# Kernel tuning notes

Measured on AMD Instinct MI355X. Metric: run time of the kernel, lower is better.

The kernel has to match this reference:

```python
import jax, jax.numpy as jnp
import numpy as np

TEMPERATURE = 0.1


def _l2norm(x):
    return x / jnp.linalg.norm(x, axis=1, keepdims=True)


def _unif(x, t=2.0):
    # torch.pdist(x).pow(2) == squared euclidean distances over pairs i<j
    m = x.shape[0]
    sq = jnp.sum(x * x, axis=1)
    d2 = sq[:, None] + sq[None, :] - 2.0 * (x @ x.T)  # [m, m]
    d2 = jnp.maximum(d2, 0.0)
    iu = jnp.triu(jnp.ones((m, m), dtype=bool), k=1)
    s = jnp.sum(jnp.where(iu, jnp.exp(-t * d2), 0.0))
    n_pairs = m * (m - 1) // 2
    return jnp.log(s / n_pairs)


def setup_inputs() -> dict:
    key = jax.random.key(0)
    k1, k2 = jax.random.split(key)
    proj_1 = jax.random.normal(k1, (4096, 1024), dtype=jnp.float32)
    proj_2 = jax.random.normal(k2, (4096, 1024), dtype=jnp.float32)
    return {"proj_1": proj_1, "proj_2": proj_2}


def reference(proj_1, proj_2):
    n = proj_1.shape[0]
    t = TEMPERATURE
    z_i = _l2norm(proj_1)
    z_j = _l2norm(proj_2)
    z = jnp.concatenate([z_i, z_j], axis=0)  # [2n, d]
    # rows are unit-norm, so cosine similarity == dot product
    sim = z @ z.T  # [2n, 2n]
    # diag(sim, +n) == diag(sim, -n) == rowwise z_i . z_j
    pos = jnp.sum(z_i * z_j, axis=1)  # [n]
    positives = jnp.concatenate([pos, pos], axis=0)  # [2n]
    mask = 1.0 - jnp.eye(2 * n, dtype=sim.dtype)
    denom = jnp.sum(mask * jnp.exp(sim / t), axis=1)  # [2n]
    # -log(exp(pos/t) / denom) == log(denom) - pos/t
    loss = jnp.sum(jnp.log(denom) - positives / t) / (2 * n)
    # alignment: mean ||z_i - z_j||_2^2 (alpha=2), detached
    lalign = jax.lax.stop_gradient(jnp.mean(jnp.sum((z_i - z_j) ** 2, axis=1)))
    # uniformity on the two halves of z_i, detached
    lunif = jax.lax.stop_gradient(
        (_unif(z_i[: n // 2]) + _unif(z_i[n // 2 :])) / 2.0
    )
    return (loss, lalign, lunif)
```

## Files before the change

### kernel.cpp

```cpp
#include <hip/hip_runtime.h>
#include <stdint.h>

#define DDIM   1024
#define M_TOT  8192
#define N_ROWS 4096
#define KT     16
#define NCELL  2080
#define SLOT   16384
#define NSLOT  3
#define LDS_TOTAL (NSLOT * SLOT)

typedef __attribute__((ext_vector_type(4))) float f32x4;
typedef __attribute__((ext_vector_type(2))) long i64x2;

__device__ __forceinline__ void gload_lds16(const void* g, void* l) {
  __builtin_amdgcn_global_load_lds(
      (const __attribute__((address_space(1))) uint32_t*)g,
      (__attribute__((address_space(3))) uint32_t*)l, 16, 0, 0);
}

__global__ __launch_bounds__(256) void knorm(const float* __restrict__ p1,
                                             const float* __restrict__ p2,
                                             unsigned char* __restrict__ z8,
                                             float* __restrict__ pp,
                                             float* __restrict__ ap) {
  const int r = blockIdx.x;
  const int t = threadIdx.x;
  const int lane = t & 63, w = t >> 6;
  __shared__ float red0[4], red1[4];

  const float4 a = ((const float4*)(p1 + (size_t)r * DDIM))[t];
  const float4 b = ((const float4*)(p2 + (size_t)r * DDIM))[t];
  float s1 = a.x*a.x + a.y*a.y + a.z*a.z + a.w*a.w;
  float s2 = b.x*b.x + b.y*b.y + b.z*b.z + b.w*b.w;
  for (int off = 1; off < 64; off <<= 1) { s1 += __shfl_xor(s1, off); s2 += __shfl_xor(s2, off); }
  if (lane == 0) { red0[w] = s1; red1[w] = s2; }
  __syncthreads();
  const float S1 = red0[0] + red0[1] + red0[2] + red0[3];
  const float S2 = red1[0] + red1[1] + red1[2] + red1[3];
  const float r1 = 1.0f / sqrtf(S1);
  const float r2 = 1.0f / sqrtf(S2);
  const float n1x = a.x*r1, n1y = a.y*r1, n1z = a.z*r1, n1w = a.w*r1;
  const float n2x = b.x*r2, n2y = b.y*r2, n2z = b.z*r2, n2w = b.w*r2;
  float pos = n1x*n2x + n1y*n2y + n1z*n2z + n1w*n2w;
  float al  = (n1x-n2x)*(n1x-n2x) + (n1y-n2y)*(n1y-n2y)
            + (n1z-n2z)*(n1z-n2z) + (n1w-n2w)*(n1w-n2w);
  __syncthreads();
  for (int off = 1; off < 64; off <<= 1) { pos += __shfl_xor(pos, off); al += __shfl_xor(al, off); }
  if (lane == 0) { red0[w] = pos; red1[w] = al; }
  __syncthreads();
  if (t == 0) {
    pp[r] = red0[0] + red0[1] + red0[2] + red0[3];
    ap[r] = red1[0] + red1[1] + red1[2] + red1[3];
  }
  const int g = t >> 4, c = (t >> 1) & 7, h = t & 1;
  const int sp = (c < 4) ? (2 * c) : (2 * (c - 4) + 1);
  const int off = g * 64 + sp * 8 + h * 4;
  int w1 = __builtin_amdgcn_cvt_pk_fp8_f32(n1x, n1y, 0, false);
  w1     = __builtin_amdgcn_cvt_pk_fp8_f32(n1z, n1w, w1, true);
  int w2 = __builtin_amdgcn_cvt_pk_fp8_f32(n2x, n2y, 0, false);
  w2     = __builtin_amdgcn_cvt_pk_fp8_f32(n2z, n2w, w2, true);
  *(int*)(z8 + (size_t)r * 1024 + off) = w1;
  *(int*)(z8 + (size_t)(r + N_ROWS) * 1024 + off) = w2;
}

__device__ __forceinline__ void stage64(const char* zb, int rowA0, int colB0,
                                        int kt, char* slot, int wid, int lane) {
  const int kb = kt * 64 + (lane >> 4) * 16;
  const int rowin = lane & 15;
  const int u0 = wid * 2, u1 = wid * 2 + 1;
  gload_lds16(zb + (size_t)(rowA0 + u0 * 16 + rowin) * 1024 + kb, slot + u0 * 1024 + lane * 16);
  gload_lds16(zb + (size_t)(rowA0 + u1 * 16 + rowin) * 1024 + kb, slot + u1 * 1024 + lane * 16);
  gload_lds16(zb + (size_t)(colB0 + u0 * 16 + rowin) * 1024 + kb, slot + 8192 + u0 * 1024 + lane * 16);
  gload_lds16(zb + (size_t)(colB0 + u1 * 16 + rowin) * 1024 + kb, slot + 8192 + u1 * 1024 + lane * 16);
}

__global__ __launch_bounds__(256, 3) void kgemm(const unsigned char* __restrict__ z,
                                                float* __restrict__ denom,
                                                float* __restrict__ uacc) {
  extern __shared__ char lds[];
  const int tid  = threadIdx.x;
  const int lane = tid & 63, wid = tid >> 6;
  const int wsr  = wid >> 1, wsc = wid & 1;
  const int lr = lane >> 4, lc = lane & 15;
  const char* zb = (const char*)z;
  const float RK10 = 14.426950408889634f;
  const float K4   = 5.770780163555856f;

  const int cdx = (blockIdx.x & 7) * 260 + (blockIdx.x >> 3);
  int SI = (int)((sqrtf(16.0f + 128.0f * (float)cdx) - 4.0f) * (1.0f / 64.0f));
  while (32 * (SI + 1) * (SI + 1) + 4 * (SI + 1) <= cdx) ++SI;
  while (32 * SI * SI + 4 * SI > cdx) --SI;
  int rem = cdx - (32 * SI * SI + 4 * SI);
  int I, J;
  if (rem < 36) {
    int ii = (int)((sqrtf(8.0f * (float)rem + 1.0f) - 1.0f) * 0.5f);
    while ((ii + 1) * (ii + 2) / 2 <= rem) ++ii;
    while (ii * (ii + 1) / 2 > rem) --ii;
    const int jj = rem - ii * (ii + 1) / 2;
    I = SI * 8 + ii; J = SI * 8 + jj;
  } else {
    const int r2 = rem - 36;
    const int SJ = r2 >> 6, w = r2 & 63;
    I = SI * 8 + (w >> 3); J = SJ * 8 + (w & 7);
  }
  const int rowA0 = I * 128, colB0 = J * 128;
  const bool useful = (colB0 + wsc * 64) < (rowA0 + wsr * 64 + 64);

  f32x4 acc[4][4] = {};

  stage64(zb, rowA0, colB0, 0, lds, wid, lane);
  stage64(zb, rowA0, colB0, 1, lds + SLOT, wid, lane);
  asm volatile("s_waitcnt vmcnt(4)" ::: "memory");
  __builtin_amdgcn_s_barrier();
  __builtin_amdgcn_sched_barrier(0);

#pragma unroll 1
  for (int t = 0; t < KT; ++t) {
    if (t + 2 < KT)
      stage64(zb, rowA0, colB0, t + 2, lds + ((t + 2) % 3) * SLOT, wid, lane);
    __builtin_amdgcn_sched_barrier(0);
    const char* S = lds + (t % 3) * SLOT;
    if (useful) {
      const char* Ab = S + wsr * 4096 + lr * 256 + lc * 16;
      const char* Bb = S + 8192 + wsc * 4096 + lr * 256 + lc * 16;
      i64x2 af[4], bg[4];
#pragma unroll
      for (int m = 0; m < 4; ++m) {
        af[m] = *(const i64x2*)(Ab + m * 1024);
        bg[m] = *(const i64x2*)(Bb + m * 1024);
      }
      __builtin_amdgcn_s_setprio(1);
#pragma unroll
      for (int q = 0; q < 2; ++q)
#pragma unroll
        for (int m = 0; m < 4; ++m)
#pragma unroll
          for (int n = 0; n < 4; ++n)
            acc[m][n] = __builtin_amdgcn_mfma_f32_16x16x32_fp8_fp8(
                af[m][q], bg[n][q], acc[m][n], 0, 0, 0);
      __builtin_amdgcn_s_setprio(0);
    }
    if (t + 2 < KT) asm volatile("s_waitcnt vmcnt(4)" ::: "memory");
    else            asm volatile("s_waitcnt vmcnt(0)" ::: "memory");
    __builtin_amdgcn_s_barrier();
    __builtin_amdgcn_sched_barrier(0);
  }

  const bool unif = (I < 16) || (I < 32 && J >= 16);
  if (useful) {
    float cs[4] = {0.0f, 0.0f, 0.0f, 0.0f};
    float u = 0.0f;
#pragma unroll
    for (int m = 0; m < 4; ++m) {
      const int growb = rowA0 + wsr * 64 + m * 16 + lr * 4;
#pragma unroll
      for (int i = 0; i < 4; ++i) {
        const int grow = growb + i;
        float rs = 0.0f;
#pragma unroll
        for (int n = 0; n < 4; ++n) {
          const int gcol = colB0 + wsc * 64 + n * 16 + lc;
          const bool incl = (gcol < grow);
          float e = incl ? exp2f(acc[m][n][i] * RK10) : 0.0f;
          rs += e;
          cs[n] += e;
          if (unif) u += incl ? exp2f(acc[m][n][i] * K4 - K4) : 0.0f;
        }
        rs += __shfl_xor(rs, 1); rs += __shfl_xor(rs, 2);
        rs += __shfl_xor(rs, 4); rs += __shfl_xor(rs, 8);
        if (lc == 0 && rs > 0.0f) atomicAdd(&denom[grow], rs);
      }
    }
#pragma unroll
    for (int n = 0; n < 4; ++n) {
      float cv = cs[n];
      cv += __shfl_xor(cv, 16); cv += __shfl_xor(cv, 32);
      if (lr == 0 && cv > 0.0f) atomicAdd(&denom[colB0 + wsc * 64 + n * 16 + lc], cv);
    }
    if (unif) {
      for (int off = 1; off < 64; off <<= 1) u += __shfl_xor(u, off);
      if (lane == 0 && u > 0.0f)
        atomicAdd(&uacc[((I < 16) ? 0 : 64) + (blockIdx.x & 63)], 2.0f * u);
    }
  }
}

__global__ __launch_bounds__(1024) void klogf(const float* __restrict__ denom,
                                              const float* __restrict__ pp,
                                              const float* __restrict__ ap,
                                              const float* __restrict__ uacc,
                                              float* __restrict__ out) {
  __shared__ float redl[16], redp[16], reda[16], ured[2];
  const int tid = threadIdx.x;
  float s = 0.0f, sp = 0.0f, sa = 0.0f;
#pragma unroll
  for (int q = 0; q < 8; ++q) s += logf(denom[q * 1024 + tid]);
#pragma unroll
  for (int q = 0; q < 4; ++q) { sp += pp[q * 1024 + tid]; sa += ap[q * 1024 + tid]; }
  const int lane = tid & 63, w = tid >> 6;
  for (int off = 1; off < 64; off <<= 1) {
    s += __shfl_xor(s, off); sp += __shfl_xor(sp, off); sa += __shfl_xor(sa, off);
  }
  if (lane == 0) { redl[w] = s; redp[w] = sp; reda[w] = sa; }
  if (tid < 64) {
    float u0 = uacc[tid], u1 = uacc[64 + tid];
    for (int off = 1; off < 64; off <<= 1) { u0 += __shfl_xor(u0, off); u1 += __shfl_xor(u1, off); }
    if (tid == 0) { ured[0] = u0; ured[1] = u1; }
  }
  __syncthreads();
  if (tid == 0) {
    float S = 0.0f, SP = 0.0f, SA = 0.0f;
#pragma unroll
    for (int i = 0; i < 16; ++i) { S += redl[i]; SP += redp[i]; SA += reda[i]; }
    const float P = 2048.0f * 2047.0f * 0.5f;
    out[0] = (S - 20.0f * SP) / 8192.0f;
    out[1] = SA / 4096.0f;
    out[2] = 0.5f * (logf(ured[0] * 0.5f / P) + logf(ured[1] * 0.5f / P));
  }
}

extern "C" void kernel_launch(void* const* d_in, const int* in_sizes, int n_in,
                              void* d_out, int out_size, void* d_ws, size_t ws_size,
                              hipStream_t stream) {
  const float* p1 = (const float*)d_in[0];
  const float* p2 = (const float*)d_in[1];
  float* out = (float*)d_out;
  char* ws = (char*)d_ws;
  unsigned char* z8 = (unsigned char*)ws;
  float* denom = (float*)(ws + (size_t)M_TOT * DDIM);
  float* uacc  = denom + M_TOT;
  float* pp    = uacc + 128;
  float* ap    = pp + 4096;

  (void)hipFuncSetAttribute((const void*)kgemm,
                            hipFuncAttributeMaxDynamicSharedMemorySize, LDS_TOTAL);
  hipMemsetAsync(denom, 0, (M_TOT + 128) * sizeof(float), stream);
  knorm<<<N_ROWS, 256, 0, stream>>>(p1, p2, z8, pp, ap);
  kgemm<<<NCELL, 256, LDS_TOTAL, stream>>>(z8, denom, uacc);
  klogf<<<1, 1024, 0, stream>>>(denom, pp, ap, uacc, out);
}
```

Baseline: 97.21 us.

## Widen GEMM tile to 128x256 with 64x128 warp subtiles

The block tile grows from 128x128 to 128x256 columns, so each warp computes a 64x128 subtile with 32 accumulators, and the lower-triangle block enumeration is rewritten for the new tile shape (1056 cells). This raises MFMA work per LDS fragment load and cuts the number of blocks and redundant A-tile loads. In exchange it needs more LDS per slot and more registers, and occupancy drops to 2 blocks per CU. Diagonal tiles also waste more work in the masked triangle.

```diff
diff --git a/kernel.cpp b/kernel.cpp
--- a/kernel.cpp
+++ b/kernel.cpp
@@ -5,8 +5,8 @@
 #define M_TOT  8192
 #define N_ROWS 4096
 #define KT     16
-#define NCELL  2080
-#define SLOT   16384
+#define NCELL  1056
+#define SLOT   24576
 #define NSLOT  3
 #define LDS_TOTAL (NSLOT * SLOT)
 
@@ -68,14 +68,18 @@
                                         int kt, char* slot, int wid, int lane) {
   const int kb = kt * 64 + (lane >> 4) * 16;
   const int rowin = lane & 15;
-  const int u0 = wid * 2, u1 = wid * 2 + 1;
-  gload_lds16(zb + (size_t)(rowA0 + u0 * 16 + rowin) * 1024 + kb, slot + u0 * 1024 + lane * 16);
-  gload_lds16(zb + (size_t)(rowA0 + u1 * 16 + rowin) * 1024 + kb, slot + u1 * 1024 + lane * 16);
-  gload_lds16(zb + (size_t)(colB0 + u0 * 16 + rowin) * 1024 + kb, slot + 8192 + u0 * 1024 + lane * 16);
-  gload_lds16(zb + (size_t)(colB0 + u1 * 16 + rowin) * 1024 + kb, slot + 8192 + u1 * 1024 + lane * 16);
-}
-
-__global__ __launch_bounds__(256, 3) void kgemm(const unsigned char* __restrict__ z,
+  const int a0 = wid * 2, a1 = wid * 2 + 1;
+  gload_lds16(zb + (size_t)(rowA0 + a0 * 16 + rowin) * 1024 + kb, slot + a0 * 1024 + lane * 16);
+  gload_lds16(zb + (size_t)(rowA0 + a1 * 16 + rowin) * 1024 + kb, slot + a1 * 1024 + lane * 16);
+#pragma unroll
+  for (int q = 0; q < 4; ++q) {
+    const int u = wid * 4 + q;
+    gload_lds16(zb + (size_t)(colB0 + u * 16 + rowin) * 1024 + kb,
+                slot + 8192 + u * 1024 + lane * 16);
+  }
+}
+
+__global__ __launch_bounds__(256, 2) void kgemm(const unsigned char* __restrict__ z,
                                                 float* __restrict__ denom,
                                                 float* __restrict__ uacc) {
   extern __shared__ char lds[];
@@ -87,31 +91,20 @@
   const float RK10 = 14.426950408889634f;
   const float K4   = 5.770780163555856f;
 
-  const int cdx = (blockIdx.x & 7) * 260 + (blockIdx.x >> 3);
-  int SI = (int)((sqrtf(16.0f + 128.0f * (float)cdx) - 4.0f) * (1.0f / 64.0f));
-  while (32 * (SI + 1) * (SI + 1) + 4 * (SI + 1) <= cdx) ++SI;
-  while (32 * SI * SI + 4 * SI > cdx) --SI;
-  int rem = cdx - (32 * SI * SI + 4 * SI);
-  int I, J;
-  if (rem < 36) {
-    int ii = (int)((sqrtf(8.0f * (float)rem + 1.0f) - 1.0f) * 0.5f);
-    while ((ii + 1) * (ii + 2) / 2 <= rem) ++ii;
-    while (ii * (ii + 1) / 2 > rem) --ii;
-    const int jj = rem - ii * (ii + 1) / 2;
-    I = SI * 8 + ii; J = SI * 8 + jj;
-  } else {
-    const int r2 = rem - 36;
-    const int SJ = r2 >> 6, w = r2 & 63;
-    I = SI * 8 + (w >> 3); J = SJ * 8 + (w & 7);
-  }
-  const int rowA0 = I * 128, colB0 = J * 128;
-  const bool useful = (colB0 + wsc * 64) < (rowA0 + wsr * 64 + 64);
-
-  f32x4 acc[4][4] = {};
+  const int c = (blockIdx.x & 7) * 132 + (blockIdx.x >> 3);
+  int I = (int)(2.0f * sqrtf((float)c + 1.0f));
+  if (I > 63) I = 63;
+  while (I < 63 && ((I + 1) * (I + 1)) / 4 + (I + 2) / 2 <= c) ++I;
+  while (I > 0 && (I * I) / 4 + (I + 1) / 2 > c) --I;
+  const int J = c - ((I * I) / 4 + (I + 1) / 2);
+  const int rowA0 = I * 128, colB0 = J * 256;
+  const bool useful = (colB0 + wsc * 128) < (rowA0 + wsr * 64 + 64);
+
+  f32x4 acc[4][8] = {};
 
   stage64(zb, rowA0, colB0, 0, lds, wid, lane);
   stage64(zb, rowA0, colB0, 1, lds + SLOT, wid, lane);
-  asm volatile("s_waitcnt vmcnt(4)" ::: "memory");
+  asm volatile("s_waitcnt vmcnt(6)" ::: "memory");
   __builtin_amdgcn_s_barrier();
   __builtin_amdgcn_sched_barrier(0);
 
@@ -123,33 +116,32 @@
     const char* S = lds + (t % 3) * SLOT;
     if (useful) {
       const char* Ab = S + wsr * 4096 + lr * 256 + lc * 16;
-      const char* Bb = S + 8192 + wsc * 4096 + lr * 256 + lc * 16;
-      i64x2 af[4], bg[4];
-#pragma unroll
-      for (int m = 0; m < 4; ++m) {
-        af[m] = *(const i64x2*)(Ab + m * 1024);
-        bg[m] = *(const i64x2*)(Bb + m * 1024);
-      }
+      const char* Bb = S + 8192 + wsc * 8192 + lr * 256 + lc * 16;
+      i64x2 af[4], bg[8];
+#pragma unroll
+      for (int m = 0; m < 4; ++m) af[m] = *(const i64x2*)(Ab + m * 1024);
+#pragma unroll
+      for (int n = 0; n < 8; ++n) bg[n] = *(const i64x2*)(Bb + n * 1024);
       __builtin_amdgcn_s_setprio(1);
 #pragma unroll
       for (int q = 0; q < 2; ++q)
 #pragma unroll
         for (int m = 0; m < 4; ++m)
 #pragma unroll
-          for (int n = 0; n < 4; ++n)
+          for (int n = 0; n < 8; ++n)
             acc[m][n] = __builtin_amdgcn_mfma_f32_16x16x32_fp8_fp8(
                 af[m][q], bg[n][q], acc[m][n], 0, 0, 0);
       __builtin_amdgcn_s_setprio(0);
     }
-    if (t + 2 < KT) asm volatile("s_waitcnt vmcnt(4)" ::: "memory");
+    if (t + 2 < KT) asm volatile("s_waitcnt vmcnt(6)" ::: "memory");
     else            asm volatile("s_waitcnt vmcnt(0)" ::: "memory");
     __builtin_amdgcn_s_barrier();
     __builtin_amdgcn_sched_barrier(0);
   }
 
-  const bool unif = (I < 16) || (I < 32 && J >= 16);
+  const bool unif = (I < 16) || (I < 32 && J >= 8);
   if (useful) {
-    float cs[4] = {0.0f, 0.0f, 0.0f, 0.0f};
+    float cs[8] = {};
     float u = 0.0f;
 #pragma unroll
     for (int m = 0; m < 4; ++m) {
@@ -159,8 +151,8 @@
         const int grow = growb + i;
         float rs = 0.0f;
 #pragma unroll
-        for (int n = 0; n < 4; ++n) {
-          const int gcol = colB0 + wsc * 64 + n * 16 + lc;
+        for (int n = 0; n < 8; ++n) {
+          const int gcol = colB0 + wsc * 128 + n * 16 + lc;
           const bool incl = (gcol < grow);
           float e = incl ? exp2f(acc[m][n][i] * RK10) : 0.0f;
           rs += e;
@@ -173,10 +165,10 @@
       }
     }
 #pragma unroll
-    for (int n = 0; n < 4; ++n) {
+    for (int n = 0; n < 8; ++n) {
       float cv = cs[n];
       cv += __shfl_xor(cv, 16); cv += __shfl_xor(cv, 32);
-      if (lr == 0 && cv > 0.0f) atomicAdd(&denom[colB0 + wsc * 64 + n * 16 + lc], cv);
+      if (lr == 0 && cv > 0.0f) atomicAdd(&denom[colB0 + wsc * 128 + n * 16 + lc], cv);
     }
     if (unif) {
       for (int off = 1; off < 64; off <<= 1) u += __shfl_xor(u, off);
```

Measured after the change: 104.7 us. 1.08x slower.

## Switch GEMM to 32x32x64 scaled FP8 MFMA with matching LDS layout

Applied to the files above, without the earlier changes.

Replaces the 16x16x32 FP8 MFMA tiles with the gfx950 mfma_scale 32x32x64 f8f6f4 instruction, using unit scales (0x7F exponent), so each wave issues 4 larger MFMAs per k-step instead of 32 small ones. The FP8 write in the normalization kernel becomes a plain linear layout, and the global-to-LDS staging and fragment loads are reorganized for 32-row blocks. The epilogue is remapped to the 32x32 accumulator layout, with wider row reductions and fewer column shuffles. The aim is higher matrix-core throughput and fewer LDS reads and instruction issues. The cost is higher accumulator register pressure per instruction and possible LDS bank conflicts in the new read pattern.

```diff
diff --git a/kernel.cpp b/kernel.cpp
--- a/kernel.cpp
+++ b/kernel.cpp
@@ -10,8 +10,10 @@
 #define NSLOT  3
 #define LDS_TOTAL (NSLOT * SLOT)
 
-typedef __attribute__((ext_vector_type(4))) float f32x4;
-typedef __attribute__((ext_vector_type(2))) long i64x2;
+typedef __attribute__((ext_vector_type(4)))  float f32x4;
+typedef __attribute__((ext_vector_type(16))) float f32x16;
+typedef __attribute__((ext_vector_type(4)))  int   i32x4;
+typedef __attribute__((ext_vector_type(8)))  int   i32x8;
 
 __device__ __forceinline__ void gload_lds16(const void* g, void* l) {
   __builtin_amdgcn_global_load_lds(
@@ -53,26 +55,27 @@
     pp[r] = red0[0] + red0[1] + red0[2] + red0[3];
     ap[r] = red1[0] + red1[1] + red1[2] + red1[3];
   }
-  const int g = t >> 4, c = (t >> 1) & 7, h = t & 1;
-  const int sp = (c < 4) ? (2 * c) : (2 * (c - 4) + 1);
-  const int off = g * 64 + sp * 8 + h * 4;
   int w1 = __builtin_amdgcn_cvt_pk_fp8_f32(n1x, n1y, 0, false);
   w1     = __builtin_amdgcn_cvt_pk_fp8_f32(n1z, n1w, w1, true);
   int w2 = __builtin_amdgcn_cvt_pk_fp8_f32(n2x, n2y, 0, false);
   w2     = __builtin_amdgcn_cvt_pk_fp8_f32(n2z, n2w, w2, true);
-  *(int*)(z8 + (size_t)r * 1024 + off) = w1;
-  *(int*)(z8 + (size_t)(r + N_ROWS) * 1024 + off) = w2;
+  *(int*)(z8 + (size_t)r * 1024 + t * 4) = w1;
+  *(int*)(z8 + (size_t)(r + N_ROWS) * 1024 + t * 4) = w2;
 }
 
 __device__ __forceinline__ void stage64(const char* zb, int rowA0, int colB0,
                                         int kt, char* slot, int wid, int lane) {
-  const int kb = kt * 64 + (lane >> 4) * 16;
-  const int rowin = lane & 15;
-  const int u0 = wid * 2, u1 = wid * 2 + 1;
-  gload_lds16(zb + (size_t)(rowA0 + u0 * 16 + rowin) * 1024 + kb, slot + u0 * 1024 + lane * 16);
-  gload_lds16(zb + (size_t)(rowA0 + u1 * 16 + rowin) * 1024 + kb, slot + u1 * 1024 + lane * 16);
-  gload_lds16(zb + (size_t)(colB0 + u0 * 16 + rowin) * 1024 + kb, slot + 8192 + u0 * 1024 + lane * 16);
-  gload_lds16(zb + (size_t)(colB0 + u1 * 16 + rowin) * 1024 + kb, slot + 8192 + u1 * 1024 + lane * 16);
+  const int r32 = lane & 31;
+  const int kc  = kt * 64 + (lane >> 5) * 32;
+#pragma unroll
+  for (int q = 0; q < 2; ++q) {
+    const int u  = wid * 2 + q;
+    const int mb = u >> 1, h = u & 1;
+    gload_lds16(zb + (size_t)(rowA0 + mb * 32 + r32) * 1024 + kc + h * 16,
+                slot + u * 1024 + lane * 16);
+    gload_lds16(zb + (size_t)(colB0 + mb * 32 + r32) * 1024 + kc + h * 16,
+                slot + 8192 + u * 1024 + lane * 16);
+  }
 }
 
 __global__ __launch_bounds__(256, 3) void kgemm(const unsigned char* __restrict__ z,
@@ -82,7 +85,7 @@
   const int tid  = threadIdx.x;
   const int lane = tid & 63, wid = tid >> 6;
   const int wsr  = wid >> 1, wsc = wid & 1;
-  const int lr = lane >> 4, lc = lane & 15;
+  const int l31  = lane & 31, hi = lane >> 5;
   const char* zb = (const char*)z;
   const float RK10 = 14.426950408889634f;
   const float K4   = 5.770780163555856f;
@@ -107,7 +110,7 @@
   const int rowA0 = I * 128, colB0 = J * 128;
   const bool useful = (colB0 + wsc * 64) < (rowA0 + wsr * 64 + 64);
 
-  f32x4 acc[4][4] = {};
+  f32x16 acc[2][2] = {};
 
   stage64(zb, rowA0, colB0, 0, lds, wid, lane);
   stage64(zb, rowA0, colB0, 1, lds + SLOT, wid, lane);
@@ -122,23 +125,26 @@
     __builtin_amdgcn_sched_barrier(0);
     const char* S = lds + (t % 3) * SLOT;
     if (useful) {
-      const char* Ab = S + wsr * 4096 + lr * 256 + lc * 16;
-      const char* Bb = S + 8192 + wsc * 4096 + lr * 256 + lc * 16;
-      i64x2 af[4], bg[4];
-#pragma unroll
-      for (int m = 0; m < 4; ++m) {
-        af[m] = *(const i64x2*)(Ab + m * 1024);
-        bg[m] = *(const i64x2*)(Bb + m * 1024);
+      const char* Ab = S + wsr * 4096 + lane * 16;
+      const char* Bb = S + 8192 + wsc * 4096 + lane * 16;
+      i32x8 a8[2], b8[2];
+#pragma unroll
+      for (int m = 0; m < 2; ++m) {
+        const i32x4 alo = *(const i32x4*)(Ab + m * 2048);
+        const i32x4 ahi = *(const i32x4*)(Ab + m * 2048 + 1024);
+        a8[m] = __builtin_shufflevector(alo, ahi, 0, 1, 2, 3, 4, 5, 6, 7);
+        const i32x4 blo = *(const i32x4*)(Bb + m * 2048);
+        const i32x4 bhi = *(const i32x4*)(Bb + m * 2048 + 1024);
+        b8[m] = __builtin_shufflevector(blo, bhi, 0, 1, 2, 3, 4, 5, 6, 7);
       }
       __builtin_amdgcn_s_setprio(1);
 #pragma unroll
-      for (int q = 0; q < 2; ++q)
-#pragma unroll
-        for (int m = 0; m < 4; ++m)
-#pragma unroll
-          for (int n = 0; n < 4; ++n)
-            acc[m][n] = __builtin_amdgcn_mfma_f32_16x16x32_fp8_fp8(
-                af[m][q], bg[n][q], acc[m][n], 0, 0, 0);
+      for (int m = 0; m < 2; ++m)
+#pragma unroll
+        for (int n = 0; n < 2; ++n)
+          acc[m][n] = __builtin_amdgcn_mfma_scale_f32_32x32x64_f8f6f4(
+              a8[m], b8[n], acc[m][n], 0, 0,
+              0, 0x7F7F7F7F, 0, 0x7F7F7F7F);
       __builtin_amdgcn_s_setprio(0);
     }
     if (t + 2 < KT) asm volatile("s_waitcnt vmcnt(4)" ::: "memory");
@@ -149,34 +155,34 @@
 
   const bool unif = (I < 16) || (I < 32 && J >= 16);
   if (useful) {
-    float cs[4] = {0.0f, 0.0f, 0.0f, 0.0f};
+    float csv[2] = {0.0f, 0.0f};
     float u = 0.0f;
 #pragma unroll
-    for (int m = 0; m < 4; ++m) {
-      const int growb = rowA0 + wsr * 64 + m * 16 + lr * 4;
-#pragma unroll
-      for (int i = 0; i < 4; ++i) {
-        const int grow = growb + i;
+    for (int mb = 0; mb < 2; ++mb) {
+#pragma unroll
+      for (int r = 0; r < 16; ++r) {
+        const int grow = rowA0 + wsr * 64 + mb * 32 + (r & 3) + 8 * (r >> 2) + 4 * hi;
         float rs = 0.0f;
 #pragma unroll
-        for (int n = 0; n < 4; ++n) {
-          const int gcol = colB0 + wsc * 64 + n * 16 + lc;
+        for (int nb = 0; nb < 2; ++nb) {
+          const int gcol = colB0 + wsc * 64 + nb * 32 + l31;
           const bool incl = (gcol < grow);
-          float e = incl ? exp2f(acc[m][n][i] * RK10) : 0.0f;
+          float e = incl ? exp2f(acc[mb][nb][r] * RK10) : 0.0f;
           rs += e;
-          cs[n] += e;
-          if (unif) u += incl ? exp2f(acc[m][n][i] * K4 - K4) : 0.0f;
+          csv[nb] += e;
+          if (unif) u += incl ? exp2f(acc[mb][nb][r] * K4 - K4) : 0.0f;
         }
-        rs += __shfl_xor(rs, 1); rs += __shfl_xor(rs, 2);
-        rs += __shfl_xor(rs, 4); rs += __shfl_xor(rs, 8);
-        if (lc == 0 && rs > 0.0f) atomicAdd(&denom[grow], rs);
+        rs += __shfl_xor(rs, 1); rs += __shfl_xor(rs, 2); rs += __shfl_xor(rs, 4);
+        rs += __shfl_xor(rs, 8); rs += __shfl_xor(rs, 16);
+        if (l31 == 0 && rs > 0.0f) atomicAdd(&denom[grow], rs);
       }
     }
 #pragma unroll
-    for (int n = 0; n < 4; ++n) {
-      float cv = cs[n];
-      cv += __shfl_xor(cv, 16); cv += __shfl_xor(cv, 32);
-      if (lr == 0 && cv > 0.0f) atomicAdd(&denom[colB0 + wsc * 64 + n * 16 + lc], cv);
+    for (int nb = 0; nb < 2; ++nb) {
+      float cv = csv[nb];
+      cv += __shfl_xor(cv, 32);
+      if (hi == 0 && cv > 0.0f)
+        atomicAdd(&denom[colB0 + wsc * 64 + nb * 32 + l31], cv);
     }
     if (unif) {
       for (int off = 1; off < 64; off <<= 1) u += __shfl_xor(u, off);
```

Result: slower. 112.1 us (+15.4%).

## Load FP8 GEMM operands directly from global memory instead of LDS pipeline

Applied to the files above, without the earlier changes.

Removes the triple-buffered LDS staging (global_load_lds, barriers, waitcnt) in the symmetric GEMM kernel and has each wave read its A/B fragments straight from global memory into registers, with a partially unrolled K loop. This eliminates LDS traffic and block-wide barriers and lets non-useful waves skip all loads. In exchange every wave fetches its own fragments with no sharing across waves, which doubles global/L2 traffic, and latency hiding now depends on unrolling and occupancy rather than an explicit prefetch pipeline.

```diff
diff --git a/kernel.cpp b/kernel.cpp
--- a/kernel.cpp
+++ b/kernel.cpp
@@ -6,18 +6,9 @@
 #define N_ROWS 4096
 #define KT     16
 #define NCELL  2080
-#define SLOT   16384
-#define NSLOT  3
-#define LDS_TOTAL (NSLOT * SLOT)
 
 typedef __attribute__((ext_vector_type(4))) float f32x4;
 typedef __attribute__((ext_vector_type(2))) long i64x2;
-
-__device__ __forceinline__ void gload_lds16(const void* g, void* l) {
-  __builtin_amdgcn_global_load_lds(
-      (const __attribute__((address_space(1))) uint32_t*)g,
-      (__attribute__((address_space(3))) uint32_t*)l, 16, 0, 0);
-}
 
 __global__ __launch_bounds__(256) void knorm(const float* __restrict__ p1,
                                              const float* __restrict__ p2,
@@ -64,21 +55,9 @@
   *(int*)(z8 + (size_t)(r + N_ROWS) * 1024 + off) = w2;
 }
 
-__device__ __forceinline__ void stage64(const char* zb, int rowA0, int colB0,
-                                        int kt, char* slot, int wid, int lane) {
-  const int kb = kt * 64 + (lane >> 4) * 16;
-  const int rowin = lane & 15;
-  const int u0 = wid * 2, u1 = wid * 2 + 1;
-  gload_lds16(zb + (size_t)(rowA0 + u0 * 16 + rowin) * 1024 + kb, slot + u0 * 1024 + lane * 16);
-  gload_lds16(zb + (size_t)(rowA0 + u1 * 16 + rowin) * 1024 + kb, slot + u1 * 1024 + lane * 16);
-  gload_lds16(zb + (size_t)(colB0 + u0 * 16 + rowin) * 1024 + kb, slot + 8192 + u0 * 1024 + lane * 16);
-  gload_lds16(zb + (size_t)(colB0 + u1 * 16 + rowin) * 1024 + kb, slot + 8192 + u1 * 1024 + lane * 16);
-}
-
 __global__ __launch_bounds__(256, 3) void kgemm(const unsigned char* __restrict__ z,
                                                 float* __restrict__ denom,
                                                 float* __restrict__ uacc) {
-  extern __shared__ char lds[];
   const int tid  = threadIdx.x;
   const int lane = tid & 63, wid = tid >> 6;
   const int wsr  = wid >> 1, wsc = wid & 1;
@@ -109,28 +88,23 @@
 
   f32x4 acc[4][4] = {};
 
-  stage64(zb, rowA0, colB0, 0, lds, wid, lane);
-  stage64(zb, rowA0, colB0, 1, lds + SLOT, wid, lane);
-  asm volatile("s_waitcnt vmcnt(4)" ::: "memory");
-  __builtin_amdgcn_s_barrier();
-  __builtin_amdgcn_sched_barrier(0);
-
-#pragma unroll 1
-  for (int t = 0; t < KT; ++t) {
-    if (t + 2 < KT)
-      stage64(zb, rowA0, colB0, t + 2, lds + ((t + 2) % 3) * SLOT, wid, lane);
-    __builtin_amdgcn_sched_barrier(0);
-    const char* S = lds + (t % 3) * SLOT;
-    if (useful) {
-      const char* Ab = S + wsr * 4096 + lr * 256 + lc * 16;
-      const char* Bb = S + 8192 + wsc * 4096 + lr * 256 + lc * 16;
+  if (useful) {
+    int aoff[4], boff[4];
+#pragma unroll
+    for (int m = 0; m < 4; ++m)
+      aoff[m] = (rowA0 + wsr * 64 + m * 16 + lc) * 1024 + lr * 16;
+#pragma unroll
+    for (int n = 0; n < 4; ++n)
+      boff[n] = (colB0 + wsc * 64 + n * 16 + lc) * 1024 + lr * 16;
+
+#pragma unroll 4
+    for (int t = 0; t < KT; ++t) {
+      const int kb = t * 64;
       i64x2 af[4], bg[4];
 #pragma unroll
-      for (int m = 0; m < 4; ++m) {
-        af[m] = *(const i64x2*)(Ab + m * 1024);
-        bg[m] = *(const i64x2*)(Bb + m * 1024);
-      }
-      __builtin_amdgcn_s_setprio(1);
+      for (int m = 0; m < 4; ++m) af[m] = *(const i64x2*)(zb + aoff[m] + kb);
+#pragma unroll
+      for (int n = 0; n < 4; ++n) bg[n] = *(const i64x2*)(zb + boff[n] + kb);
 #pragma unroll
       for (int q = 0; q < 2; ++q)
 #pragma unroll
@@ -139,12 +113,7 @@
           for (int n = 0; n < 4; ++n)
             acc[m][n] = __builtin_amdgcn_mfma_f32_16x16x32_fp8_fp8(
                 af[m][q], bg[n][q], acc[m][n], 0, 0, 0);
-      __builtin_amdgcn_s_setprio(0);
-    }
-    if (t + 2 < KT) asm volatile("s_waitcnt vmcnt(4)" ::: "memory");
-    else            asm volatile("s_waitcnt vmcnt(0)" ::: "memory");
-    __builtin_amdgcn_s_barrier();
-    __builtin_amdgcn_sched_barrier(0);
+    }
   }
 
   const bool unif = (I < 16) || (I < 32 && J >= 16);
@@ -233,10 +202,8 @@
   float* pp    = uacc + 128;
   float* ap    = pp + 4096;
 
-  (void)hipFuncSetAttribute((const void*)kgemm,
-                            hipFuncAttributeMaxDynamicSharedMemorySize, LDS_TOTAL);
   hipMemsetAsync(denom, 0, (M_TOT + 128) * sizeof(float), stream);
   knorm<<<N_ROWS, 256, 0, stream>>>(p1, p2, z8, pp, ap);
-  kgemm<<<NCELL, 256, LDS_TOTAL, stream>>>(z8, denom, uacc);
+  kgemm<<<NCELL, 256, 0, stream>>>(z8, denom, uacc);
   klogf<<<1, 1024, 0, stream>>>(denom, pp, ap, uacc, out);
 }
```

Result: slower. 156.0 us (+60.5%).
